# Optimization experiments

Hardware: AMD Instinct MI355X
Metric: run time of the kernel (lower is better)

Reference implementation:

```python
import jax, jax.numpy as jnp
import numpy as np

N = 8192
NFEAT = 256
NHID = 64


def setup_inputs() -> dict:
    key = jax.random.key(0)
    k1, k2, k3, k4, k5 = jax.random.split(key, 5)
    x = jax.random.normal(k1, (N, NFEAT), dtype=jnp.float32)
    # symmetric-normalized-ish dense adjacency (random sparse-like weights)
    adj = jax.random.uniform(k2, (N, N), dtype=jnp.float32)
    W1 = jax.random.normal(k3, (NFEAT, NHID), dtype=jnp.float32) * (1.0 / np.sqrt(NFEAT))
    W2 = jax.random.normal(k4, (NHID, NHID), dtype=jnp.float32) * (1.0 / np.sqrt(NHID))
    W3 = jax.random.normal(k5, (NHID, NHID), dtype=jnp.float32) * (1.0 / np.sqrt(NHID))
    return {"x": x, "adj": adj, "W1": W1, "W2": W2, "W3": W3}


def _gcn(x, adj, W):
    # eval mode: dropout is identity. support = x @ W ; out = adj @ support
    return adj @ (x @ W)


def reference(x, adj, W1, W2, W3):
    h1 = jax.nn.relu(_gcn(x, adj, W1))         # [N, nhid]
    mu = _gcn(h1, adj, W2)                      # [N, nhid]
    logvar = _gcn(h1, adj, W3)                  # [N, nhid]
    z = mu                                      # eval: reparameterize returns mu
    recon = z @ z.T                             # [N, N] inner-product decode, act=identity
    return recon, mu, logvar
```

## Files before the change

kernel.cpp:

```cpp
#include <hip/hip_runtime.h>

typedef __bf16 bf16;
typedef __attribute__((ext_vector_type(4))) __bf16 bf16x4;
typedef __attribute__((ext_vector_type(8))) __bf16 bf16x8;
typedef __attribute__((ext_vector_type(4))) float f32x4;

#define MFMA16(a, b, c) __builtin_amdgcn_mfma_f32_16x16x32_bf16((a), (b), (c), 0, 0, 0)

constexpr int N   = 8192;
constexpr int HID = 64;

template <int EPI>
__global__ __launch_bounds__(256) void gcn_pass(const float* __restrict__ A, int K,
                                                const bf16* __restrict__ Bt,
                                                bf16* __restrict__ outT,
                                                const bf16* __restrict__ W23T,
                                                float* __restrict__ mu,
                                                float* __restrict__ lv) {
  __shared__ bf16  As[4][2][16 * 64];
  __shared__ float Hred[4][16][68];
  __shared__ float Ht[16][72];
  const int tid = threadIdx.x, lane = tid & 63, w = tid >> 6;
  const int r = lane & 15, hi = lane >> 4;
  const int i0 = blockIdx.x * 16;
  const int Kw = K >> 2;
  const int kb0 = w * Kw;
  const int nt = Kw / 64;
  const int aR = hi;
  const int aC = r * 4;

  float4 ra[4][4];
  bf16x8 rb[2][8];
  f32x4 acc[4] = {};

  auto loadA = [&](float4 (&dst)[4], int t) {
    const int k0 = kb0 + t * 64;
#pragma unroll
    for (int s = 0; s < 4; ++s)
      dst[s] = *reinterpret_cast<const float4*>(&A[(size_t)(i0 + 4 * s + aR) * K + k0 + aC]);
  };
  auto loadB = [&](bf16x8 (&dst)[8], int t) {
    const int k0 = kb0 + t * 64;
#pragma unroll
    for (int n = 0; n < 4; ++n)
#pragma unroll
      for (int kk = 0; kk < 2; ++kk)
        dst[n * 2 + kk] = *reinterpret_cast<const bf16x8*>(
            &Bt[(size_t)(n * 16 + r) * K + k0 + kk * 32 + hi * 8]);
  };
  auto writeA = [&](int buf, const float4 (&src)[4]) {
    char* base = (char*)&As[w][buf][0];
#pragma unroll
    for (int s = 0; s < 4; ++s) {
      const int R = 4 * s + aR;
      bf16x4 o;
      o[0] = (bf16)src[s].x; o[1] = (bf16)src[s].y;
      o[2] = (bf16)src[s].z; o[3] = (bf16)src[s].w;
      *reinterpret_cast<bf16x4*>(base + R * 128 + ((aC * 2) ^ ((R & 7) << 4))) = o;
    }
  };
  auto compute = [&](int buf, const bf16x8 (&rbv)[8]) {
    const char* base = (const char*)&As[w][buf][0];
#pragma unroll
    for (int kk = 0; kk < 2; ++kk) {
      const bf16x8 fa = *reinterpret_cast<const bf16x8*>(
          base + r * 128 + ((kk * 64 + hi * 16) ^ ((r & 7) << 4)));
#pragma unroll
      for (int n = 0; n < 4; ++n)
        acc[n] = MFMA16(fa, rbv[n * 2 + kk], acc[n]);
    }
  };

  loadA(ra[0], 0);
  if (nt > 1) loadA(ra[1], 1);
  if (nt > 2) loadA(ra[2], 2);
  if (nt > 3) loadA(ra[3], 3);
  loadB(rb[0], 0);
  writeA(0, ra[0]);

  for (int tb = 0; tb < nt; tb += 4) {
#pragma unroll
    for (int u = 0; u < 4; ++u) {
      const int t = tb + u;
      if (t >= nt) continue;
      if (t + 1 < nt) {
        writeA((u + 1) & 1, ra[(u + 1) & 3]);
        loadB(rb[(u + 1) & 1], t + 1);
      }
      if (t + 4 < nt) loadA(ra[u & 3], t + 4);
      compute(u & 1, rb[u & 1]);
    }
  }

#pragma unroll
  for (int n = 0; n < 4; ++n)
#pragma unroll
    for (int g = 0; g < 4; ++g)
      Hred[w][hi * 4 + g][n * 16 + r] = acc[n][g];
  __syncthreads();
  {
    const int row = tid >> 4, c4 = (tid & 15) * 4;
    float4 s = {0.f, 0.f, 0.f, 0.f};
#pragma unroll
    for (int q = 0; q < 4; ++q) {
      const float4 v = *reinterpret_cast<const float4*>(&Hred[q][row][c4]);
      s.x += v.x; s.y += v.y; s.z += v.z; s.w += v.w;
    }
    if (EPI == 1) {
      s.x = fmaxf(s.x, 0.f); s.y = fmaxf(s.y, 0.f);
      s.z = fmaxf(s.z, 0.f); s.w = fmaxf(s.w, 0.f);
    }
    *reinterpret_cast<float4*>(&Ht[row][c4]) = s;
  }
  __syncthreads();

  if constexpr (EPI <= 1) {
    const int j = tid >> 2, iq = tid & 3;
    bf16x4 o;
#pragma unroll
    for (int e = 0; e < 4; ++e) o[e] = (bf16)Ht[iq * 4 + e][j];
    *reinterpret_cast<bf16x4*>(&outT[(size_t)j * N + i0 + iq * 4]) = o;
  } else {
    f32x4 a2[2] = {};
#pragma unroll
    for (int kk = 0; kk < 2; ++kk) {
      const float4 t0 = *reinterpret_cast<const float4*>(&Ht[r][kk * 32 + hi * 8]);
      const float4 t1 = *reinterpret_cast<const float4*>(&Ht[r][kk * 32 + hi * 8 + 4]);
      bf16x8 fa;
      fa[0] = (bf16)t0.x; fa[1] = (bf16)t0.y; fa[2] = (bf16)t0.z; fa[3] = (bf16)t0.w;
      fa[4] = (bf16)t1.x; fa[5] = (bf16)t1.y; fa[6] = (bf16)t1.z; fa[7] = (bf16)t1.w;
#pragma unroll
      for (int j = 0; j < 2; ++j) {
        const int q = w * 2 + j;
        const bf16x8 fw = *reinterpret_cast<const bf16x8*>(
            &W23T[(size_t)(q * 16 + r) * 64 + kk * 32 + hi * 8]);
        a2[j] = MFMA16(fa, fw, a2[j]);
      }
    }
#pragma unroll
    for (int j = 0; j < 2; ++j) {
      const int q = w * 2 + j;
      float* dst = (q < 4) ? mu : lv;
      const int cc = (q & 3) * 16 + r;
#pragma unroll
      for (int g = 0; g < 4; ++g)
        dst[(size_t)(i0 + hi * 4 + g) * HID + cc] = a2[j][g];
    }
  }
}

__global__ void prep_w1t(const float* __restrict__ W1, bf16* __restrict__ W1T) {
  const int idx = blockIdx.x * 256 + threadIdx.x;
  const int j = idx >> 8, k = idx & 255;
  W1T[idx] = (bf16)W1[k * HID + j];
}

__global__ void prep_w23t(const float* __restrict__ W2, const float* __restrict__ W3,
                          bf16* __restrict__ Wt) {
  const int idx = blockIdx.x * 256 + threadIdx.x;
  const int j = idx >> 6, c = idx & 63;
  Wt[idx] = (bf16)(j < 64 ? W2[c * HID + j] : W3[c * HID + (j - 64)]);
}

constexpr int LDT = 72;
__global__ __launch_bounds__(256) void recon_mm(const float* __restrict__ mu,
                                                float* __restrict__ out) {
  __shared__ bf16 Am[128 * LDT];
  __shared__ bf16 Bm[128 * LDT];
  const int tid = threadIdx.x, lane = tid & 63, wave = tid >> 6;
  const int i0 = blockIdx.x * 128, j0 = blockIdx.y * 128;
  {
    const int rr = tid >> 4, c4 = tid & 15;
#pragma unroll
    for (int s = 0; s < 8; ++s) {
      const int row = rr + s * 16;
      const float4 v = *reinterpret_cast<const float4*>(&mu[(size_t)(i0 + row) * HID + c4 * 4]);
      bf16x4 o;
      o[0] = (bf16)v.x; o[1] = (bf16)v.y; o[2] = (bf16)v.z; o[3] = (bf16)v.w;
      *reinterpret_cast<bf16x4*>(&Am[row * LDT + c4 * 4]) = o;
      const float4 u = *reinterpret_cast<const float4*>(&mu[(size_t)(j0 + row) * HID + c4 * 4]);
      bf16x4 p;
      p[0] = (bf16)u.x; p[1] = (bf16)u.y; p[2] = (bf16)u.z; p[3] = (bf16)u.w;
      *reinterpret_cast<bf16x4*>(&Bm[row * LDT + c4 * 4]) = p;
    }
  }
  __syncthreads();
  f32x4 acc[2][8] = {};
  const int rA = wave * 32 + (lane & 15);
#pragma unroll
  for (int kk = 0; kk < 2; ++kk) {
    const int kb = kk * 32 + ((lane >> 4) << 3);
    const bf16x8 a0 = *reinterpret_cast<const bf16x8*>(&Am[rA * LDT + kb]);
    const bf16x8 a1 = *reinterpret_cast<const bf16x8*>(&Am[(rA + 16) * LDT + kb]);
#pragma unroll
    for (int n = 0; n < 8; ++n) {
      const bf16x8 b = *reinterpret_cast<const bf16x8*>(&Bm[(n * 16 + (lane & 15)) * LDT + kb]);
      acc[0][n] = MFMA16(a0, b, acc[0][n]);
      acc[1][n] = MFMA16(a1, b, acc[1][n]);
    }
  }
  const int r4 = (lane >> 4) << 2, c = lane & 15;
#pragma unroll
  for (int m = 0; m < 2; ++m)
#pragma unroll
    for (int n = 0; n < 8; ++n)
#pragma unroll
      for (int g = 0; g < 4; ++g)
        out[(size_t)(i0 + wave * 32 + m * 16 + r4 + g) * N + j0 + n * 16 + c] = acc[m][n][g];
}

extern "C" void kernel_launch(void* const* d_in, const int* in_sizes, int n_in, void* d_out,
                              int out_size, void* d_ws, size_t ws_size, hipStream_t stream) {
  const float* x   = (const float*)d_in[0];
  const float* adj = (const float*)d_in[1];
  const float* W1  = (const float*)d_in[2];
  const float* W2  = (const float*)d_in[3];
  const float* W3  = (const float*)d_in[4];

  float* out    = (float*)d_out;
  float* recon  = out;
  float* mu_out = out + (size_t)N * N;
  float* lv_out = mu_out + (size_t)N * HID;

  char* scr   = (char*)d_out;
  bf16* S1T   = (bf16*)(scr + 0);
  bf16* h1T   = (bf16*)(scr + (1u << 20));
  bf16* W1T   = (bf16*)(scr + (2u << 20));
  bf16* W23T  = (bf16*)(scr + (2u << 20) + 65536);

  prep_w1t<<<64, 256, 0, stream>>>(W1, W1T);
  prep_w23t<<<32, 256, 0, stream>>>(W2, W3, W23T);
  gcn_pass<0><<<512, 256, 0, stream>>>(x, 256, W1T, S1T, nullptr, nullptr, nullptr);
  gcn_pass<1><<<512, 256, 0, stream>>>(adj, N, S1T, h1T, nullptr, nullptr, nullptr);
  gcn_pass<2><<<512, 256, 0, stream>>>(adj, N, h1T, nullptr, W23T, mu_out, lv_out);
  recon_mm<<<dim3(64, 64), 256, 0, stream>>>(mu_out, recon);
}
```

Baseline: 246.5 us.

## Deepen A prefetch, stage recon output through LDS, merge weight prep kernels

Raises the register prefetch depth for the streamed adjacency tiles in the GCN passes from four to six tiles, to keep more global loads in flight. Stages the recon tile through shared memory so each row is written with coalesced float4 stores instead of scattered scalar stores. Merges the two weight-transpose kernels into one launch. The trade-off is extra register pressure in the GCN kernel, which may cut occupancy, and two extra barriers in recon.

```diff
diff --git a/kernel.cpp b/kernel.cpp
--- a/kernel.cpp
+++ b/kernel.cpp
@@ -29,7 +29,7 @@
   const int aR = hi;
   const int aC = r * 4;
 
-  float4 ra[4][4];
+  float4 ra[6][4];
   bf16x8 rb[2][8];
   f32x4 acc[4] = {};
 
@@ -75,19 +75,21 @@
   if (nt > 1) loadA(ra[1], 1);
   if (nt > 2) loadA(ra[2], 2);
   if (nt > 3) loadA(ra[3], 3);
+  if (nt > 4) loadA(ra[4], 4);
+  if (nt > 5) loadA(ra[5], 5);
   loadB(rb[0], 0);
   writeA(0, ra[0]);
 
-  for (int tb = 0; tb < nt; tb += 4) {
-#pragma unroll
-    for (int u = 0; u < 4; ++u) {
+  for (int tb = 0; tb < nt; tb += 6) {
+#pragma unroll
+    for (int u = 0; u < 6; ++u) {
       const int t = tb + u;
       if (t >= nt) continue;
       if (t + 1 < nt) {
-        writeA((u + 1) & 1, ra[(u + 1) & 3]);
+        writeA((u + 1) & 1, ra[(u + 1) % 6]);
         loadB(rb[(u + 1) & 1], t + 1);
       }
-      if (t + 4 < nt) loadA(ra[u & 3], t + 4);
+      if (t + 6 < nt) loadA(ra[u % 6], t + 6);
       compute(u & 1, rb[u & 1]);
     }
   }
@@ -149,24 +151,27 @@
   }
 }
 
-__global__ void prep_w1t(const float* __restrict__ W1, bf16* __restrict__ W1T) {
+__global__ void prep_weights(const float* __restrict__ W1, const float* __restrict__ W2,
+                             const float* __restrict__ W3, bf16* __restrict__ W1T,
+                             bf16* __restrict__ W23T) {
   const int idx = blockIdx.x * 256 + threadIdx.x;
-  const int j = idx >> 8, k = idx & 255;
-  W1T[idx] = (bf16)W1[k * HID + j];
-}
-
-__global__ void prep_w23t(const float* __restrict__ W2, const float* __restrict__ W3,
-                          bf16* __restrict__ Wt) {
-  const int idx = blockIdx.x * 256 + threadIdx.x;
-  const int j = idx >> 6, c = idx & 63;
-  Wt[idx] = (bf16)(j < 64 ? W2[c * HID + j] : W3[c * HID + (j - 64)]);
+  if (idx < 16384) {
+    const int j = idx >> 8, k = idx & 255;
+    W1T[idx] = (bf16)W1[k * HID + j];
+  } else {
+    const int g = idx - 16384;
+    const int j = g >> 6, c = g & 63;
+    W23T[g] = (bf16)(j < 64 ? W2[c * HID + j] : W3[c * HID + (j - 64)]);
+  }
 }
 
 constexpr int LDT = 72;
 __global__ __launch_bounds__(256) void recon_mm(const float* __restrict__ mu,
                                                 float* __restrict__ out) {
-  __shared__ bf16 Am[128 * LDT];
-  __shared__ bf16 Bm[128 * LDT];
+  __shared__ alignas(16) char pool[128 * LDT * 2 * 2];
+  bf16* Am = (bf16*)pool;
+  bf16* Bm = (bf16*)(pool + 128 * LDT * 2);
+  float* Ct = (float*)pool;
   const int tid = threadIdx.x, lane = tid & 63, wave = tid >> 6;
   const int i0 = blockIdx.x * 128, j0 = blockIdx.y * 128;
   {
@@ -201,12 +206,27 @@
   }
   const int r4 = (lane >> 4) << 2, c = lane & 15;
 #pragma unroll
-  for (int m = 0; m < 2; ++m)
-#pragma unroll
-    for (int n = 0; n < 8; ++n)
-#pragma unroll
-      for (int g = 0; g < 4; ++g)
-        out[(size_t)(i0 + wave * 32 + m * 16 + r4 + g) * N + j0 + n * 16 + c] = acc[m][n][g];
+  for (int h = 0; h < 2; ++h) {
+    __syncthreads();
+    if ((wave >> 1) == h) {
+      const int rbase = (wave & 1) * 32;
+#pragma unroll
+      for (int m = 0; m < 2; ++m)
+#pragma unroll
+        for (int n = 0; n < 8; ++n)
+#pragma unroll
+          for (int g = 0; g < 4; ++g)
+            Ct[(rbase + m * 16 + r4 + g) * 132 + n * 16 + c] = acc[m][n][g];
+    }
+    __syncthreads();
+#pragma unroll
+    for (int s = 0; s < 8; ++s) {
+      const int idx = tid + s * 256;
+      const int row = idx >> 5, q = idx & 31;
+      const float4 v = *reinterpret_cast<const float4*>(&Ct[row * 132 + q * 4]);
+      *reinterpret_cast<float4*>(&out[(size_t)(i0 + h * 64 + row) * N + j0 + q * 4]) = v;
+    }
+  }
 }
 
 extern "C" void kernel_launch(void* const* d_in, const int* in_sizes, int n_in, void* d_out,
@@ -228,8 +248,7 @@
   bf16* W1T   = (bf16*)(scr + (2u << 20));
   bf16* W23T  = (bf16*)(scr + (2u << 20) + 65536);
 
-  prep_w1t<<<64, 256, 0, stream>>>(W1, W1T);
-  prep_w23t<<<32, 256, 0, stream>>>(W2, W3, W23T);
+  prep_weights<<<96, 256, 0, stream>>>(W1, W2, W3, W1T, W23T);
   gcn_pass<0><<<512, 256, 0, stream>>>(x, 256, W1T, S1T, nullptr, nullptr, nullptr);
   gcn_pass<1><<<512, 256, 0, stream>>>(adj, N, S1T, h1T, nullptr, nullptr, nullptr);
   gcn_pass<2><<<512, 256, 0, stream>>>(adj, N, h1T, nullptr, W23T, mu_out, lv_out);
```

After: 245.7 us. About the same (-0.3%).
